# Kernel optimization log

Hardware: AMD Instinct MI355X
Metric: run time of the kernel (lower is better)

## Reference

```python
import jax, jax.numpy as jnp
import numpy as np

B, T, D_IN, H, G = 64, 512, 862, 1024, 4096  # G = 4*H, PyTorch gate order i,f,g,o


def setup_inputs() -> dict:
    key = jax.random.key(0)
    ks = jax.random.split(key, 9)
    s0 = 1.0 / np.sqrt(H)  # PyTorch LSTM init scale
    return {
        "x": jax.random.normal(ks[0], (B, T, D_IN), dtype=jnp.float32),
        "W_ih0": jax.random.normal(ks[1], (G, D_IN), dtype=jnp.float32) * s0,
        "W_hh0": jax.random.normal(ks[2], (G, H), dtype=jnp.float32) * s0,
        "b_ih0": jax.random.normal(ks[3], (G,), dtype=jnp.float32) * s0,
        "b_hh0": jax.random.normal(ks[4], (G,), dtype=jnp.float32) * s0,
        "W_ih1": jax.random.normal(ks[5], (G, H), dtype=jnp.float32) * s0,
        "W_hh1": jax.random.normal(ks[6], (G, H), dtype=jnp.float32) * s0,
        "b_ih1": jax.random.normal(ks[7], (G,), dtype=jnp.float32) * s0,
        "b_hh1": jax.random.normal(ks[8], (G,), dtype=jnp.float32) * s0,
    }


def _lstm_layer(x, W_ih, W_hh, b_ih, b_hh):
    # x: [B, T, D]; gates precomputed for the input projection (one big GEMM)
    b, t, _ = x.shape
    h_dim = W_hh.shape[1]
    xg = jnp.einsum("btd,gd->btg", x, W_ih) + (b_ih + b_hh)  # [B, T, 4H]

    def step(carry, xt):
        h, c = carry
        g = xt + h @ W_hh.T  # [B, 4H]
        i, f, gc, o = jnp.split(g, 4, axis=-1)  # PyTorch order i,f,g,o
        i = jax.nn.sigmoid(i)
        f = jax.nn.sigmoid(f)
        gc = jnp.tanh(gc)
        o = jax.nn.sigmoid(o)
        c = f * c + i * gc
        h = o * jnp.tanh(c)
        return (h, c), h

    h0 = jnp.zeros((b, h_dim), x.dtype)
    c0 = jnp.zeros((b, h_dim), x.dtype)
    _, hs = jax.lax.scan(step, (h0, c0), jnp.swapaxes(xg, 0, 1))  # [T, B, H]
    return jnp.swapaxes(hs, 0, 1)  # [B, T, H]


def reference(x, W_ih0, W_hh0, b_ih0, b_hh0, W_ih1, W_hh1, b_ih1, b_hh1):
    h1 = _lstm_layer(x, W_ih0, W_hh0, b_ih0, b_hh0)
    out = _lstm_layer(h1, W_ih1, W_hh1, b_ih1, b_hh1)
    return out
```

## Files before the change

kernel.cpp:

```cpp
#include <hip/hip_runtime.h>
#include <cstdint>

#define BATCH 64
#define SEQ   512
#define DIN   862
#define DPAD  896
#define HID   1024
#define NG    4096

typedef _Float16 f16;
typedef __attribute__((ext_vector_type(8))) _Float16 f16x8;
typedef __attribute__((ext_vector_type(4))) float    f32x4;
typedef unsigned long long u64;

__device__ __forceinline__ void glds16(const f16* g, f16* l) {
    auto gp = (const __attribute__((address_space(1))) void*)(uintptr_t)g;
    auto lp = (__attribute__((address_space(3))) void*)(uint32_t)(uintptr_t)l;
    __builtin_amdgcn_global_load_lds(gp, lp, 16, 0, 0);
}

__device__ __forceinline__ float sigf(float x) {
    return __builtin_amdgcn_rcpf(1.f + __expf(-x));
}
__device__ __forceinline__ float tanh_fast(float x) {
    float xx = fminf(15.f, fmaxf(-15.f, x));
    float e = __expf(2.f * xx);
    return (e - 1.f) * __builtin_amdgcn_rcpf(e + 1.f);
}

__device__ __forceinline__ long xg_index(int t, int b, int n) {
    int bs = b >> 4, bl = b & 15;
    int g = n >> 10, jh = n & 1023;
    int jg = jh >> 4, jl = jh & 15;
    return (((((long)t * 4 + bs) * 64 + jg) * 4 + g) * 16 + bl) * 16 + jl;
}

__device__ __forceinline__ f16x8 h_frag_load(const f16* p) {
    union { u64 u[2]; f16x8 v; } r;
    r.u[0] = __hip_atomic_load((u64*)p,     __ATOMIC_RELAXED, __HIP_MEMORY_SCOPE_AGENT);
    r.u[1] = __hip_atomic_load((u64*)p + 1, __ATOMIC_RELAXED, __HIP_MEMORY_SCOPE_AGENT);
    return r.v;
}

__global__ __launch_bounds__(256) void prep_kernel(
    const float* __restrict__ x,
    const float* __restrict__ Wih0, const float* __restrict__ Whh0,
    const float* __restrict__ bih0, const float* __restrict__ bhh0,
    const float* __restrict__ Wih1, const float* __restrict__ Whh1,
    const float* __restrict__ bih1, const float* __restrict__ bhh1,
    f16* __restrict__ xh, f16* __restrict__ W0h, f16* __restrict__ Wh0h,
    f16* __restrict__ W1h, f16* __restrict__ Wh1h,
    float* __restrict__ b0, float* __restrict__ b1, unsigned* __restrict__ bar)
{
    long tid = (long)blockIdx.x * blockDim.x + threadIdx.x;
    long np  = (long)gridDim.x * blockDim.x;
    for (long i = tid; i < (long)BATCH * SEQ * DPAD; i += np) {
        long m = i / DPAD, k = i % DPAD;
        xh[i] = (k < DIN) ? (f16)x[m * DIN + k] : (f16)0.f;
    }
    for (long i = tid; i < (long)NG * DPAD; i += np) {
        long n = i / DPAD, k = i % DPAD;
        W0h[i] = (k < DIN) ? (f16)Wih0[n * DIN + k] : (f16)0.f;
    }
    for (long i = tid; i < (long)NG * HID; i += np) {
        Wh0h[i] = (f16)Whh0[i];
        W1h[i]  = (f16)Wih1[i];
        Wh1h[i] = (f16)Whh1[i];
    }
    for (long i = tid; i < NG; i += np) { b0[i] = bih0[i] + bhh0[i]; b1[i] = bih1[i] + bhh1[i]; }
    for (long i = tid; i < 2048; i += np) bar[i] = 0u;
}

__global__ __launch_bounds__(256) void gemm_f16(
    const f16* __restrict__ A, const f16* __restrict__ Bw,
    const float* __restrict__ bias, f16* __restrict__ out, int K, int mode)
{
    __shared__ f16 smem[2 * 128 * 32];
    const int tid  = threadIdx.x;
    const int lane = tid & 63, wave = tid >> 6;
    const int wm = wave >> 1, wn = wave & 1;
    const int quad = lane >> 4, l15 = lane & 15;
    const int bm = blockIdx.x >> 5, bn = blockIdx.x & 31;
    const long m0 = (long)bm * 128, n0 = (long)bn * 128;
    const int r4 = lane >> 2, g4 = lane & 3;

    f32x4 acc[4][4];
#pragma unroll
    for (int i = 0; i < 4; ++i)
#pragma unroll
        for (int j = 0; j < 4; ++j)
#pragma unroll
            for (int r = 0; r < 4; ++r) acc[i][j][r] = 0.f;

#pragma unroll 1
    for (int kk = 0; kk < K; kk += 32) {
#pragma unroll
        for (int c = 0; c < 2; ++c) {
            int idx = wave * 2 + c;
            int lr  = idx * 16 + r4;
            int gs  = g4 ^ ((lr >> 1) & 3);
            glds16(A  + (m0 + lr) * (long)K + kk + gs * 8, smem + idx * 512);
            glds16(Bw + (n0 + lr) * (long)K + kk + gs * 8, smem + 4096 + idx * 512);
        }
        __syncthreads();
        f16x8 af[4], bf[4];
#pragma unroll
        for (int i = 0; i < 4; ++i) {
            int lr = 64 * wm + 16 * i + l15;
            int sl = quad ^ ((lr >> 1) & 3);
            af[i] = *(const f16x8*)(smem + lr * 32 + sl * 8);
        }
#pragma unroll
        for (int j = 0; j < 4; ++j) {
            int lr = 64 * wn + 16 * j + l15;
            int sl = quad ^ ((lr >> 1) & 3);
            bf[j] = *(const f16x8*)(smem + 4096 + lr * 32 + sl * 8);
        }
#pragma unroll
        for (int i = 0; i < 4; ++i)
#pragma unroll
            for (int j = 0; j < 4; ++j)
                acc[i][j] = __builtin_amdgcn_mfma_f32_16x16x32_f16(af[i], bf[j], acc[i][j], 0, 0, 0);
        __syncthreads();
    }

#pragma unroll
    for (int j = 0; j < 4; ++j) {
        int n = (int)n0 + 64 * wn + 16 * j + l15;
        float bv = bias[n];
#pragma unroll
        for (int i = 0; i < 4; ++i) {
#pragma unroll
            for (int r = 0; r < 4; ++r) {
                int m = (int)m0 + 64 * wm + 16 * i + quad * 4 + r;
                int t, b;
                if (mode == 1) { b = m >> 9; t = m & 511; }
                else           { t = m >> 6; b = m & 63; }
                out[xg_index(t, b, n)] = (f16)(acc[i][j][r] + bv);
            }
        }
    }
}

__device__ __forceinline__ void grid_barrier_nf(unsigned* bar, unsigned target) {
    asm volatile("s_waitcnt vmcnt(0)" ::: "memory");
    __syncthreads();
    if (threadIdx.x == 0) {
        unsigned grp = blockIdx.x >> 4;
        unsigned prev = __hip_atomic_fetch_add(&bar[grp * 32], 1u, __ATOMIC_RELAXED, __HIP_MEMORY_SCOPE_AGENT);
        if ((prev & 15u) == 15u) {
            unsigned pr = __hip_atomic_fetch_add(&bar[512], 1u, __ATOMIC_RELAXED, __HIP_MEMORY_SCOPE_AGENT);
            if ((pr & 15u) == 15u)
                __hip_atomic_store(&bar[544], target, __ATOMIC_RELAXED, __HIP_MEMORY_SCOPE_AGENT);
        }
        while (__hip_atomic_load(&bar[544], __ATOMIC_RELAXED, __HIP_MEMORY_SCOPE_AGENT) < target)
            __builtin_amdgcn_s_sleep(1);
    }
    __syncthreads();
}

__global__ __launch_bounds__(256, 1) __attribute__((amdgpu_waves_per_eu(1, 1)))
void lstm_layer(
    const f16* __restrict__ xg, const f16* __restrict__ Whh,
    f16* __restrict__ hseq, float* __restrict__ out32, unsigned* __restrict__ bar)
{
    __shared__ float P[4 * 4 * 16 * 17];
    const int tid = threadIdx.x;
    const int lane = tid & 63, w = tid >> 6;
    const int quad = lane >> 4, l15 = lane & 15;
    const int bs = blockIdx.x & 3;
    const int jg = blockIdx.x >> 2;
    const int ks0 = 256 * w;

    f16x8 wf[4][8];
#pragma unroll
    for (int g = 0; g < 4; ++g) {
        const f16* Wp = Whh + ((long)g * HID + jg * 16 + l15) * HID + ks0 + quad * 8;
#pragma unroll
        for (int s = 0; s < 8; ++s)
            wf[g][s] = *(const f16x8*)(Wp + s * 32);
    }

    const int gb = tid >> 4, gj = tid & 15;
    const int bG = bs * 16 + gb, jG = jg * 16 + gj;
    unsigned* hw = (unsigned*)hseq;
    float cst = 0.f;

#pragma unroll 1
    for (int t = 0; t < SEQ; ++t) {
#pragma unroll
        for (int g = 0; g < 4; ++g)
#pragma unroll
            for (int s = 0; s < 8; ++s)
                asm volatile("" : "+v"(wf[g][s]));

        const f16* xp = xg + (((long)t * 4 + bs) * 64 + jg) * 1024 + gb * 16 + gj;
        float xgi = (float)xp[0];
        float xgf = (float)xp[256];
        float xgg = (float)xp[512];
        float xgo = (float)xp[768];

        f32x4 acc[4];
#pragma unroll
        for (int g = 0; g < 4; ++g)
#pragma unroll
            for (int r = 0; r < 4; ++r) acc[g][r] = 0.f;

        if (t > 0) {
            const f16* hpf = hseq + ((long)(t - 1) * BATCH + bs * 16 + l15) * HID + ks0 + quad * 8;
#pragma unroll
            for (int s = 0; s < 8; ++s) {
                f16x8 af = h_frag_load(hpf + s * 32);
#pragma unroll
                for (int g = 0; g < 4; ++g)
                    acc[g] = __builtin_amdgcn_mfma_f32_16x16x32_f16(af, wf[g][s], acc[g], 0, 0, 0);
            }
        }

#pragma unroll
        for (int g = 0; g < 4; ++g)
#pragma unroll
            for (int r = 0; r < 4; ++r)
                P[((w * 4 + g) * 16 + quad * 4 + r) * 17 + l15] = acc[g][r];
        __syncthreads();

        float gate[4];
#pragma unroll
        for (int g = 0; g < 4; ++g) {
            float s0 = P[((0 * 4 + g) * 16 + gb) * 17 + gj];
            float s1 = P[((1 * 4 + g) * 16 + gb) * 17 + gj];
            float s2 = P[((2 * 4 + g) * 16 + gb) * 17 + gj];
            float s3 = P[((3 * 4 + g) * 16 + gb) * 17 + gj];
            gate[g] = (s0 + s1) + (s2 + s3);
        }

        float gi = gate[0] + xgi;
        float gf = gate[1] + xgf;
        float gg = gate[2] + xgg;
        float go = gate[3] + xgo;
        float si = sigf(gi), sf = sigf(gf), so = sigf(go);
        float tg = tanh_fast(gg);
        cst = sf * cst + si * tg;
        float h = so * tanh_fast(cst);

        union { f16 f; unsigned short u; } cv; cv.f = (f16)h;
        unsigned hv = cv.u;
        unsigned ov = __shfl_xor(hv, 1);
        if (!(tid & 1))
            __hip_atomic_store(&hw[(((long)t * BATCH + bG) * HID + jG) >> 1],
                               hv | (ov << 16), __ATOMIC_RELAXED, __HIP_MEMORY_SCOPE_AGENT);
        if (out32) out32[((long)bG * SEQ + t) * HID + jG] = h;

        if (t + 1 < SEQ) grid_barrier_nf(bar, (unsigned)(t + 1));
    }
}

extern "C" void kernel_launch(void* const* d_in, const int* in_sizes, int n_in,
                              void* d_out, int out_size, void* d_ws, size_t ws_size,
                              hipStream_t stream) {
    (void)in_sizes; (void)n_in; (void)out_size; (void)ws_size;
    const float* x    = (const float*)d_in[0];
    const float* Wih0 = (const float*)d_in[1];
    const float* Whh0 = (const float*)d_in[2];
    const float* bih0 = (const float*)d_in[3];
    const float* bhh0 = (const float*)d_in[4];
    const float* Wih1 = (const float*)d_in[5];
    const float* Whh1 = (const float*)d_in[6];
    const float* bih1 = (const float*)d_in[7];
    const float* bhh1 = (const float*)d_in[8];

    char* ws = (char*)d_ws;
    size_t off = 0;
    auto alloc = [&](size_t bytes) { char* p = ws + off; off += (bytes + 255) & ~(size_t)255; return p; };
    f16*   XG   = (f16*)alloc((size_t)SEQ * BATCH * NG * 2);
    f16*   xh   = (f16*)alloc((size_t)BATCH * SEQ * DPAD * 2);
    f16*   h1   = (f16*)alloc((size_t)SEQ * BATCH * HID * 2);
    f16*   W0h  = (f16*)alloc((size_t)NG * DPAD * 2);
    f16*   Wh0h = (f16*)alloc((size_t)NG * HID * 2);
    f16*   W1h  = (f16*)alloc((size_t)NG * HID * 2);
    f16*   Wh1h = (f16*)alloc((size_t)NG * HID * 2);
    float* b0   = (float*)alloc((size_t)NG * 4);
    float* b1   = (float*)alloc((size_t)NG * 4);
    unsigned* bar = (unsigned*)alloc(2048 * 4);

    prep_kernel<<<dim3(2048), dim3(256), 0, stream>>>(x, Wih0, Whh0, bih0, bhh0,
                                                      Wih1, Whh1, bih1, bhh1,
                                                      xh, W0h, Wh0h, W1h, Wh1h, b0, b1, bar);

    gemm_f16<<<dim3(8192), dim3(256), 0, stream>>>(xh, W0h, b0, XG, DPAD, 1);

    {
        const f16* xgp = XG; const f16* whp = Wh0h; f16* hp = h1;
        float* op = nullptr; unsigned* bp = bar;
        void* args[] = { (void*)&xgp, (void*)&whp, (void*)&hp, (void*)&op, (void*)&bp };
        (void)hipLaunchCooperativeKernel((const void*)lstm_layer, dim3(256), dim3(256), args, 0, stream);
    }

    gemm_f16<<<dim3(8192), dim3(256), 0, stream>>>(h1, W1h, b1, XG, HID, 2);

    {
        const f16* xgp = XG; const f16* whp = Wh1h; f16* hp = h1;
        float* op = (float*)d_out; unsigned* bp = bar + 1024;
        void* args[] = { (void*)&xgp, (void*)&whp, (void*)&hp, (void*)&op, (void*)&bp };
        (void)hipLaunchCooperativeKernel((const void*)lstm_layer, dim3(256), dim3(256), args, 0, stream);
    }
}
```

Baseline: 6.099 ms.

## Replace grid-wide barrier with per-batch-slice flag polling in LSTM recurrence

Drops the hierarchical grid barrier run every timestep. Each wave now publishes a per-wave step counter, and consumers poll only the 256 flags of their own batch slice before loading h(t-1). The LDS partial-sum buffer is double-buffered by step parity so the missing trailing barrier cannot cause a race, and layer 2 writes to its own h buffer. This cuts synchronisation latency and lets independent batch slices drift apart, but it relies on relaxed atomics plus vmcnt waits for visibility and removes the register-pinning asm and the waves_per_eu attribute.

```diff
diff --git a/kernel.cpp b/kernel.cpp
--- a/kernel.cpp
+++ b/kernel.cpp
@@ -68,7 +68,8 @@
         Wh1h[i] = (f16)Whh1[i];
     }
     for (long i = tid; i < NG; i += np) { b0[i] = bih0[i] + bhh0[i]; b1[i] = bih1[i] + bhh1[i]; }
-    for (long i = tid; i < 2048; i += np) bar[i] = 0u;
+    for (long i = tid; i < 2048; i += np)
+        __hip_atomic_store(&bar[i], 0u, __ATOMIC_RELAXED, __HIP_MEMORY_SCOPE_AGENT);
 }
 
 __global__ __launch_bounds__(256) void gemm_f16(
@@ -142,29 +143,11 @@
     }
 }
 
-__device__ __forceinline__ void grid_barrier_nf(unsigned* bar, unsigned target) {
-    asm volatile("s_waitcnt vmcnt(0)" ::: "memory");
-    __syncthreads();
-    if (threadIdx.x == 0) {
-        unsigned grp = blockIdx.x >> 4;
-        unsigned prev = __hip_atomic_fetch_add(&bar[grp * 32], 1u, __ATOMIC_RELAXED, __HIP_MEMORY_SCOPE_AGENT);
-        if ((prev & 15u) == 15u) {
-            unsigned pr = __hip_atomic_fetch_add(&bar[512], 1u, __ATOMIC_RELAXED, __HIP_MEMORY_SCOPE_AGENT);
-            if ((pr & 15u) == 15u)
-                __hip_atomic_store(&bar[544], target, __ATOMIC_RELAXED, __HIP_MEMORY_SCOPE_AGENT);
-        }
-        while (__hip_atomic_load(&bar[544], __ATOMIC_RELAXED, __HIP_MEMORY_SCOPE_AGENT) < target)
-            __builtin_amdgcn_s_sleep(1);
-    }
-    __syncthreads();
-}
-
-__global__ __launch_bounds__(256, 1) __attribute__((amdgpu_waves_per_eu(1, 1)))
-void lstm_layer(
+__global__ __launch_bounds__(256, 1) void lstm_layer(
     const f16* __restrict__ xg, const f16* __restrict__ Whh,
     f16* __restrict__ hseq, float* __restrict__ out32, unsigned* __restrict__ bar)
 {
-    __shared__ float P[4 * 4 * 16 * 17];
+    __shared__ float P[2][4 * 4 * 16 * 17];
     const int tid = threadIdx.x;
     const int lane = tid & 63, w = tid >> 6;
     const int quad = lane >> 4, l15 = lane & 15;
@@ -184,16 +167,13 @@
     const int gb = tid >> 4, gj = tid & 15;
     const int bG = bs * 16 + gb, jG = jg * 16 + gj;
     unsigned* hw = (unsigned*)hseq;
+    const unsigned* pollp = bar + bs * 256 + 64 * w + lane;
+    unsigned* sigp = bar + ((bs * 64 + jg) * 4 + w);
     float cst = 0.f;
 
 #pragma unroll 1
     for (int t = 0; t < SEQ; ++t) {
-#pragma unroll
-        for (int g = 0; g < 4; ++g)
-#pragma unroll
-            for (int s = 0; s < 8; ++s)
-                asm volatile("" : "+v"(wf[g][s]));
-
+        const int par = t & 1;
         const f16* xp = xg + (((long)t * 4 + bs) * 64 + jg) * 1024 + gb * 16 + gj;
         float xgi = (float)xp[0];
         float xgf = (float)xp[256];
@@ -207,6 +187,15 @@
             for (int r = 0; r < 4; ++r) acc[g][r] = 0.f;
 
         if (t > 0) {
+            const unsigned tgt = (unsigned)t;
+            for (;;) {
+                unsigned v = __hip_atomic_load((unsigned*)pollp,
+                                               __ATOMIC_RELAXED, __HIP_MEMORY_SCOPE_AGENT);
+                if (__all((int)(v >= tgt))) break;
+                __builtin_amdgcn_s_sleep(1);
+            }
+            __builtin_amdgcn_sched_barrier(0);
+
             const f16* hpf = hseq + ((long)(t - 1) * BATCH + bs * 16 + l15) * HID + ks0 + quad * 8;
 #pragma unroll
             for (int s = 0; s < 8; ++s) {
@@ -221,16 +210,16 @@
         for (int g = 0; g < 4; ++g)
 #pragma unroll
             for (int r = 0; r < 4; ++r)
-                P[((w * 4 + g) * 16 + quad * 4 + r) * 17 + l15] = acc[g][r];
+                P[par][((w * 4 + g) * 16 + quad * 4 + r) * 17 + l15] = acc[g][r];
         __syncthreads();
 
         float gate[4];
 #pragma unroll
         for (int g = 0; g < 4; ++g) {
-            float s0 = P[((0 * 4 + g) * 16 + gb) * 17 + gj];
-            float s1 = P[((1 * 4 + g) * 16 + gb) * 17 + gj];
-            float s2 = P[((2 * 4 + g) * 16 + gb) * 17 + gj];
-            float s3 = P[((3 * 4 + g) * 16 + gb) * 17 + gj];
+            float s0 = P[par][((0 * 4 + g) * 16 + gb) * 17 + gj];
+            float s1 = P[par][((1 * 4 + g) * 16 + gb) * 17 + gj];
+            float s2 = P[par][((2 * 4 + g) * 16 + gb) * 17 + gj];
+            float s3 = P[par][((3 * 4 + g) * 16 + gb) * 17 + gj];
             gate[g] = (s0 + s1) + (s2 + s3);
         }
 
@@ -251,7 +240,10 @@
                                hv | (ov << 16), __ATOMIC_RELAXED, __HIP_MEMORY_SCOPE_AGENT);
         if (out32) out32[((long)bG * SEQ + t) * HID + jG] = h;
 
-        if (t + 1 < SEQ) grid_barrier_nf(bar, (unsigned)(t + 1));
+        asm volatile("s_waitcnt vmcnt(0)" ::: "memory");
+        if (lane == 0)
+            __hip_atomic_store(sigp, (unsigned)(t + 1),
+                               __ATOMIC_RELAXED, __HIP_MEMORY_SCOPE_AGENT);
     }
 }
 
@@ -275,6 +267,7 @@
     f16*   XG   = (f16*)alloc((size_t)SEQ * BATCH * NG * 2);
     f16*   xh   = (f16*)alloc((size_t)BATCH * SEQ * DPAD * 2);
     f16*   h1   = (f16*)alloc((size_t)SEQ * BATCH * HID * 2);
+    f16*   h2   = (f16*)alloc((size_t)SEQ * BATCH * HID * 2);
     f16*   W0h  = (f16*)alloc((size_t)NG * DPAD * 2);
     f16*   Wh0h = (f16*)alloc((size_t)NG * HID * 2);
     f16*   W1h  = (f16*)alloc((size_t)NG * HID * 2);
@@ -299,7 +292,7 @@
     gemm_f16<<<dim3(8192), dim3(256), 0, stream>>>(h1, W1h, b1, XG, HID, 2);
 
     {
-        const f16* xgp = XG; const f16* whp = Wh1h; f16* hp = h1;
+        const f16* xgp = XG; const f16* whp = Wh1h; f16* hp = h2;
         float* op = (float*)d_out; unsigned* bp = bar + 1024;
         void* args[] = { (void*)&xgp, (void*)&whp, (void*)&hp, (void*)&op, (void*)&bp };
         (void)hipLaunchCooperativeKernel((const void*)lstm_layer, dim3(256), dim3(256), args, 0, stream);
```

Measured after the change: 6.781 ms. 11.2% more time.
